# Kernel tuning notes

Measured on AMD Instinct MI355X. Metric: run time of the kernel, lower is better.

Reference implementation:

```python
import jax, jax.numpy as jnp
import numpy as np

EMBED_DIM = 1024
NUM_HEADS = 16
HEAD_DIM = EMBED_DIM // NUM_HEADS
BATCH = 2
SEQ = 2048


def setup_inputs() -> dict:
    key = jax.random.key(0)
    k_x, k_wi, k_bi, k_wo, k_bo = jax.random.split(key, 5)
    scale_in = 1.0 / np.sqrt(EMBED_DIM)
    x = jax.random.normal(k_x, (BATCH, SEQ, EMBED_DIM), dtype=jnp.float32)
    # nn.Linear stores weight [out, in]; we keep [in, out] for x @ W.
    w_in = jax.random.uniform(k_wi, (EMBED_DIM, 3 * EMBED_DIM), jnp.float32, -scale_in, scale_in)
    b_in = jax.random.uniform(k_bi, (3 * EMBED_DIM,), jnp.float32, -scale_in, scale_in)
    w_out = jax.random.uniform(k_wo, (EMBED_DIM, EMBED_DIM), jnp.float32, -scale_in, scale_in)
    b_out = jax.random.uniform(k_bo, (EMBED_DIM,), jnp.float32, -scale_in, scale_in)
    return {"x": x, "w_in": w_in, "b_in": b_in, "w_out": w_out, "b_out": b_out}


def reference(x, w_in, b_in, w_out, b_out):
    B, S, E = x.shape
    H, D = NUM_HEADS, HEAD_DIM
    inp = x @ w_in + b_in                       # [B,S,3E]
    que, key, val = jnp.split(inp, 3, axis=-1)  # each [B,S,E]
    que = que.reshape(B, S, H, D)
    key = key.reshape(B, S, H, D)
    val = val.reshape(B, S, H, D)
    scores = jnp.einsum('bshd,brhd->bhsr', que, key) * (1.0 / np.sqrt(D))
    weights = jax.nn.softmax(scores, axis=-1)   # [B,H,S,S]
    attn = jnp.einsum('bhsr,brhd->bshd', weights, val).reshape(B, S, E)
    return attn @ w_out + b_out
```

## Files before the change

### kernel.cpp

```cpp
#include <hip/hip_runtime.h>


typedef __bf16 bf16x8 __attribute__((ext_vector_type(8)));
typedef float  f32x4  __attribute__((ext_vector_type(4)));
typedef short  s16x4  __attribute__((ext_vector_type(4)));
typedef short  s16x8  __attribute__((ext_vector_type(8)));

__device__ __forceinline__ unsigned short f2b(float f) {
  unsigned u = __float_as_uint(f);
  unsigned r = u + 0x7fffu + ((u >> 16) & 1u);
  return (unsigned short)(r >> 16);
}

__device__ __forceinline__ void gl_lds16(const void* g, void* l) {
  __builtin_amdgcn_global_load_lds(
      (__attribute__((address_space(1))) void*)g,
      (__attribute__((address_space(3))) void*)l, 16, 0, 0);
}

__device__ __forceinline__ f32x4 mfma16x16x16(s16x4 a, s16x4 b, f32x4 c) {
#if defined(__HIP_DEVICE_COMPILE__)
#if __has_builtin(__builtin_amdgcn_mfma_f32_16x16x16bf16_1k)
  return __builtin_amdgcn_mfma_f32_16x16x16bf16_1k(a, b, c, 0, 0, 0);
#else
  s16x8 a8 = {a[0], a[1], a[2], a[3], 0, 0, 0, 0};
  s16x8 b8 = {b[0], b[1], b[2], b[3], 0, 0, 0, 0};
  union U { s16x8 s; bf16x8 v; };
  U ua, ub; ua.s = a8; ub.s = b8;
  return __builtin_amdgcn_mfma_f32_16x16x32_bf16(ua.v, ub.v, c, 0, 0, 0);
#endif
#else
  (void)a; (void)b;
  return c;
#endif
}

__global__ __launch_bounds__(256) void cast_kernel(
    const float* __restrict__ in, unsigned short* __restrict__ out, int n4) {
  int i = blockIdx.x * 256 + threadIdx.x;
  if (i < n4) {
    float4 v = ((const float4*)in)[i];
    ushort4 o;
    o.x = f2b(v.x); o.y = f2b(v.y); o.z = f2b(v.z); o.w = f2b(v.w);
    ((ushort4*)out)[i] = o;
  }
}

__global__ __launch_bounds__(256) void transpose_cast_kernel(
    const float* __restrict__ in, unsigned short* __restrict__ out, int R, int C) {
  __shared__ float tile[64][65];
  int r0 = blockIdx.y * 64, c0 = blockIdx.x * 64;
  int tid = threadIdx.x;
#pragma unroll
  for (int p = 0; p < 16; p++) {
    int i = tid + p * 256;
    int ri = i >> 6, ci = i & 63;
    tile[ri][ci] = in[(size_t)(r0 + ri) * C + c0 + ci];
  }
  __syncthreads();
#pragma unroll
  for (int p = 0; p < 16; p++) {
    int i = tid + p * 256;
    int ci = i >> 6, ri = i & 63;
    out[(size_t)(c0 + ci) * R + r0 + ri] = f2b(tile[ri][ci]);
  }
}

__global__ __launch_bounds__(256) void vt_transpose_kernel(
    const unsigned short* __restrict__ qkv, unsigned short* __restrict__ vt) {
  __shared__ unsigned short tile[64][65];
  int bid = blockIdx.x;
  int st = bid & 31, h = (bid >> 5) & 15, b = bid >> 9;
  int s0 = st * 64;
  int tid = threadIdx.x;
  const unsigned short* src = qkv + (size_t)(b * 2048 + s0) * 3072 + 2048 + h * 64;
#pragma unroll
  for (int p = 0; p < 16; p++) {
    int i = tid + p * 256;
    int sr = i >> 6, d = i & 63;
    tile[sr][d] = src[(size_t)sr * 3072 + d];
  }
  __syncthreads();
  unsigned short* dst = vt + (size_t)(b * 16 + h) * 64 * 2048 + s0;
#pragma unroll
  for (int p = 0; p < 16; p++) {
    int i = tid + p * 256;
    int dr = i >> 6, sc = i & 63;
    dst[(size_t)dr * 2048 + sc] = tile[sc][dr];
  }
}

template <int OUT_BF16>
__global__ __launch_bounds__(256) void gemm_bt(
    const unsigned short* __restrict__ A, const unsigned short* __restrict__ Bt,
    const float* __restrict__ bias, void* __restrict__ Cp, int M, int N, int K,
    int qcols, float qscale) {
  __shared__ __align__(16) unsigned short As[128 * 32];
  __shared__ __align__(16) unsigned short Bs[128 * 32];
  int tid = threadIdx.x;
  int wave = tid >> 6, lane = tid & 63;
  int m_l = lane & 15, quad = lane >> 4;
  int wm = (wave >> 1) * 64, wn = (wave & 1) * 64;
  int row = tid >> 2, kp = (tid & 3) << 3;
  const unsigned short* ag = A + (size_t)(blockIdx.y * 128 + row) * K + kp;
  const unsigned short* bg = Bt + (size_t)(blockIdx.x * 128 + row) * K + kp;
  unsigned short* asw = As + wave * 512;
  unsigned short* bsw = Bs + wave * 512;
  f32x4 acc[4][4] = {};
  for (int k0 = 0; k0 < K; k0 += 32) {
    __syncthreads();
    gl_lds16(ag + k0, asw);
    gl_lds16(ag + (size_t)64 * K + k0, asw + 2048);
    gl_lds16(bg + k0, bsw);
    gl_lds16(bg + (size_t)64 * K + k0, bsw + 2048);
    __syncthreads();
    bf16x8 af[4], bf[4];
#pragma unroll
    for (int i = 0; i < 4; i++)
      af[i] = *(const bf16x8*)&As[(wm + i * 16 + m_l) * 32 + quad * 8];
#pragma unroll
    for (int j = 0; j < 4; j++)
      bf[j] = *(const bf16x8*)&Bs[(wn + j * 16 + m_l) * 32 + quad * 8];
#pragma unroll
    for (int i = 0; i < 4; i++)
#pragma unroll
      for (int j = 0; j < 4; j++)
        acc[i][j] = __builtin_amdgcn_mfma_f32_16x16x32_bf16(af[i], bf[j], acc[i][j], 0, 0, 0);
  }
  float bv[4];
#pragma unroll
  for (int j = 0; j < 4; j++) bv[j] = bias[blockIdx.x * 128 + wn + j * 16 + m_l];
#pragma unroll
  for (int i = 0; i < 4; i++) {
    int m = blockIdx.y * 128 + wm + i * 16 + quad * 4;
#pragma unroll
    for (int j = 0; j < 4; j++) {
      int n = blockIdx.x * 128 + wn + j * 16 + m_l;
      float sc = (OUT_BF16 && n < qcols) ? qscale : 1.0f;
#pragma unroll
      for (int r = 0; r < 4; r++) {
        float v = (acc[i][j][r] + bv[j]) * sc;
        if (OUT_BF16)
          ((unsigned short*)Cp)[(size_t)(m + r) * N + n] = f2b(v);
        else
          ((float*)Cp)[(size_t)(m + r) * N + n] = v;
      }
    }
  }
}

__global__ __launch_bounds__(256) void attn_kernel(
    const unsigned short* __restrict__ qkv, const unsigned short* __restrict__ vt,
    unsigned short* __restrict__ aout) {
  __shared__ __align__(16) unsigned short Qs[128 * 64];
  __shared__ __align__(16) unsigned short Ks[64 * 64];
  __shared__ __align__(16) unsigned short Vts[64 * 64];
  int bid = blockIdx.x;
  int qt = bid & 15, h = (bid >> 4) & 15, b = bid >> 8;
  int tid = threadIdx.x, wave = tid >> 6;
  int lane = tid & 63;
  int m_l = lane & 15, quad = lane >> 4;
  int q0 = qt * 128;
  const unsigned short* qb = qkv + (size_t)b * 2048 * 3072 + h * 64;
  const unsigned short* kb = qb + 1024;
  const unsigned short* vtb = vt + (size_t)(b * 16 + h) * 64 * 2048;

  int srow = tid >> 3;
  int sd0 = ((tid & 7) ^ (srow & 7)) * 8;

#pragma unroll
  for (int i = 0; i < 4; i++)
    gl_lds16(qb + (size_t)(q0 + i * 32 + srow) * 3072 + sd0,
             Qs + wave * 512 + i * 2048);
  __syncthreads();

  int sw0 = ((quad ^ (m_l & 7)) * 8);
  int sw1 = (((quad + 4) ^ (m_l & 7)) * 8);

  bf16x8 qf[2][2];
#pragma unroll
  for (int qi = 0; qi < 2; qi++) {
    int r = (wave * 32 + qi * 16 + m_l) * 64;
    qf[qi][0] = *(const bf16x8*)&Qs[r + sw0];
    qf[qi][1] = *(const bf16x8*)&Qs[r + sw1];
  }

  f32x4 o[2][4] = {};
  float lp[2] = {0.f, 0.f};

  for (int kt = 0; kt < 2048; kt += 64) {
    __syncthreads();
    gl_lds16(kb + (size_t)(kt + srow) * 3072 + sd0, Ks + wave * 512);
    gl_lds16(kb + (size_t)(kt + 32 + srow) * 3072 + sd0, Ks + 2048 + wave * 512);
    gl_lds16(vtb + (size_t)srow * 2048 + kt + sd0, Vts + wave * 512);
    gl_lds16(vtb + (size_t)(32 + srow) * 2048 + kt + sd0, Vts + 2048 + wave * 512);
    __syncthreads();

#pragma unroll
    for (int t = 0; t < 4; t++) {
      int kr = (t * 16 + m_l) * 64;
      bf16x8 kf0 = *(const bf16x8*)&Ks[kr + sw0];
      bf16x8 kf1 = *(const bf16x8*)&Ks[kr + sw1];
      s16x4 pfrag[2];
#pragma unroll
      for (int qi = 0; qi < 2; qi++) {
        f32x4 z = {};
        f32x4 s = __builtin_amdgcn_mfma_f32_16x16x32_bf16(kf0, qf[qi][0], z, 0, 0, 0);
        s = __builtin_amdgcn_mfma_f32_16x16x32_bf16(kf1, qf[qi][1], s, 0, 0, 0);
        float p0 = __builtin_exp2f(s[0]);
        float p1 = __builtin_exp2f(s[1]);
        float p2 = __builtin_exp2f(s[2]);
        float p3 = __builtin_exp2f(s[3]);
        lp[qi] += (p0 + p1) + (p2 + p3);
        s16x4 pk;
        pk[0] = (short)f2b(p0); pk[1] = (short)f2b(p1);
        pk[2] = (short)f2b(p2); pk[3] = (short)f2b(p3);
        pfrag[qi] = pk;
      }
#pragma unroll
      for (int dt = 0; dt < 4; dt++) {
        int drow = dt * 16 + m_l;
        int kchunk = (t * 2 + (quad >> 1)) ^ (m_l & 7);
        s16x4 vf = *(const s16x4*)&Vts[drow * 64 + kchunk * 8 + (quad & 1) * 4];
        o[0][dt] = mfma16x16x16(vf, pfrag[0], o[0][dt]);
        o[1][dt] = mfma16x16x16(vf, pfrag[1], o[1][dt]);
      }
    }
  }

#pragma unroll
  for (int qi = 0; qi < 2; qi++) {
    lp[qi] += __shfl_xor(lp[qi], 16, 64);
    lp[qi] += __shfl_xor(lp[qi], 32, 64);
  }

  unsigned short* ob = aout + (size_t)(b * 2048 + q0 + wave * 32 + m_l) * 1024 +
                       h * 64 + quad * 4;
#pragma unroll
  for (int qi = 0; qi < 2; qi++) {
    float rl = 1.0f / lp[qi];
#pragma unroll
    for (int dt = 0; dt < 4; dt++) {
      ushort4 w;
      w.x = f2b(o[qi][dt][0] * rl);
      w.y = f2b(o[qi][dt][1] * rl);
      w.z = f2b(o[qi][dt][2] * rl);
      w.w = f2b(o[qi][dt][3] * rl);
      *(ushort4*)&ob[(size_t)qi * 16 * 1024 + dt * 16] = w;
    }
  }
}

extern "C" void kernel_launch(void* const* d_in, const int* in_sizes, int n_in,
                              void* d_out, int out_size, void* d_ws, size_t ws_size,
                              hipStream_t stream) {
  (void)in_sizes; (void)n_in; (void)out_size; (void)ws_size;
  const float* x     = (const float*)d_in[0];
  const float* w_in  = (const float*)d_in[1];
  const float* b_in  = (const float*)d_in[2];
  const float* w_out = (const float*)d_in[3];
  const float* b_out = (const float*)d_in[4];
  char* ws = (char*)d_ws;
  unsigned short* xb    = (unsigned short*)(ws + 0);
  unsigned short* wint  = (unsigned short*)(ws + 8388608);
  unsigned short* woutt = (unsigned short*)(ws + 14680064);
  unsigned short* qkv   = (unsigned short*)(ws + 16777216);
  unsigned short* vt    = (unsigned short*)(ws + 41943040);
  unsigned short* attn  = (unsigned short*)(ws + 50331648);
  float* out = (float*)d_out;

  const float QSCALE = 0.125f * 1.44269504088896f;

  cast_kernel<<<4096, 256, 0, stream>>>(x, xb, 1048576);
  transpose_cast_kernel<<<dim3(48, 16), 256, 0, stream>>>(w_in, wint, 1024, 3072);
  transpose_cast_kernel<<<dim3(16, 16), 256, 0, stream>>>(w_out, woutt, 1024, 1024);
  gemm_bt<1><<<dim3(24, 32), 256, 0, stream>>>(xb, wint, b_in, qkv, 4096, 3072, 1024,
                                               1024, QSCALE);
  vt_transpose_kernel<<<1024, 256, 0, stream>>>(qkv, vt);
  attn_kernel<<<512, 256, 0, stream>>>(qkv, vt, attn);
  gemm_bt<0><<<dim3(8, 32), 256, 0, stream>>>(attn, woutt, b_out, out, 4096, 1024, 1024,
                                              0, 1.0f);
}
```

Baseline: 231.7 us.

## Split attention work across 8 waves and use packed bf16 conversion

The attention kernel now launches 512 threads per block, so each of the 8 waves handles 16 query rows instead of 32. K/V tile loads are spread across more threads, which halves the loads issued per thread. The software bf16 rounding is replaced with the hardware v_cvt_pk_bf16_f32 instruction for the probability fragments and the output. This should raise occupancy and latency hiding, but K fragment LDS reads are now amortised over fewer MFMAs per wave, and block-wide barriers cover twice as many waves.

```diff
diff --git a/kernel.cpp b/kernel.cpp
--- a/kernel.cpp
+++ b/kernel.cpp
@@ -10,6 +10,16 @@
   unsigned u = __float_as_uint(f);
   unsigned r = u + 0x7fffu + ((u >> 16) & 1u);
   return (unsigned short)(r >> 16);
+}
+
+__device__ __forceinline__ unsigned cvt_pk_bf16(float a, float b) {
+#if defined(__HIP_DEVICE_COMPILE__)
+  unsigned r;
+  asm("v_cvt_pk_bf16_f32 %0, %1, %2" : "=v"(r) : "v"(a), "v"(b));
+  return r;
+#else
+  return (unsigned)f2b(a) | ((unsigned)f2b(b) << 16);
+#endif
 }
 
 __device__ __forceinline__ void gl_lds16(const void* g, void* l) {
@@ -149,7 +159,7 @@
   }
 }
 
-__global__ __launch_bounds__(256) void attn_kernel(
+__global__ __launch_bounds__(512) void attn_kernel(
     const unsigned short* __restrict__ qkv, const unsigned short* __restrict__ vt,
     unsigned short* __restrict__ aout) {
   __shared__ __align__(16) unsigned short Qs[128 * 64];
@@ -168,32 +178,24 @@
   int srow = tid >> 3;
   int sd0 = ((tid & 7) ^ (srow & 7)) * 8;
 
-#pragma unroll
-  for (int i = 0; i < 4; i++)
-    gl_lds16(qb + (size_t)(q0 + i * 32 + srow) * 3072 + sd0,
-             Qs + wave * 512 + i * 2048);
+  gl_lds16(qb + (size_t)(q0 + srow) * 3072 + sd0, Qs + wave * 512);
+  gl_lds16(qb + (size_t)(q0 + 64 + srow) * 3072 + sd0, Qs + 4096 + wave * 512);
   __syncthreads();
 
   int sw0 = ((quad ^ (m_l & 7)) * 8);
   int sw1 = (((quad + 4) ^ (m_l & 7)) * 8);
 
-  bf16x8 qf[2][2];
-#pragma unroll
-  for (int qi = 0; qi < 2; qi++) {
-    int r = (wave * 32 + qi * 16 + m_l) * 64;
-    qf[qi][0] = *(const bf16x8*)&Qs[r + sw0];
-    qf[qi][1] = *(const bf16x8*)&Qs[r + sw1];
-  }
-
-  f32x4 o[2][4] = {};
-  float lp[2] = {0.f, 0.f};
+  int qrow = (wave * 16 + m_l) * 64;
+  bf16x8 qf0 = *(const bf16x8*)&Qs[qrow + sw0];
+  bf16x8 qf1 = *(const bf16x8*)&Qs[qrow + sw1];
+
+  f32x4 o[4] = {};
+  float lp = 0.f;
 
   for (int kt = 0; kt < 2048; kt += 64) {
     __syncthreads();
     gl_lds16(kb + (size_t)(kt + srow) * 3072 + sd0, Ks + wave * 512);
-    gl_lds16(kb + (size_t)(kt + 32 + srow) * 3072 + sd0, Ks + 2048 + wave * 512);
     gl_lds16(vtb + (size_t)srow * 2048 + kt + sd0, Vts + wave * 512);
-    gl_lds16(vtb + (size_t)(32 + srow) * 2048 + kt + sd0, Vts + 2048 + wave * 512);
     __syncthreads();
 
 #pragma unroll
@@ -201,53 +203,39 @@
       int kr = (t * 16 + m_l) * 64;
       bf16x8 kf0 = *(const bf16x8*)&Ks[kr + sw0];
       bf16x8 kf1 = *(const bf16x8*)&Ks[kr + sw1];
-      s16x4 pfrag[2];
-#pragma unroll
-      for (int qi = 0; qi < 2; qi++) {
-        f32x4 z = {};
-        f32x4 s = __builtin_amdgcn_mfma_f32_16x16x32_bf16(kf0, qf[qi][0], z, 0, 0, 0);
-        s = __builtin_amdgcn_mfma_f32_16x16x32_bf16(kf1, qf[qi][1], s, 0, 0, 0);
-        float p0 = __builtin_exp2f(s[0]);
-        float p1 = __builtin_exp2f(s[1]);
-        float p2 = __builtin_exp2f(s[2]);
-        float p3 = __builtin_exp2f(s[3]);
-        lp[qi] += (p0 + p1) + (p2 + p3);
-        s16x4 pk;
-        pk[0] = (short)f2b(p0); pk[1] = (short)f2b(p1);
-        pk[2] = (short)f2b(p2); pk[3] = (short)f2b(p3);
-        pfrag[qi] = pk;
-      }
+      f32x4 z = {};
+      f32x4 s = __builtin_amdgcn_mfma_f32_16x16x32_bf16(kf0, qf0, z, 0, 0, 0);
+      s = __builtin_amdgcn_mfma_f32_16x16x32_bf16(kf1, qf1, s, 0, 0, 0);
+      float p0 = __builtin_exp2f(s[0]);
+      float p1 = __builtin_exp2f(s[1]);
+      float p2 = __builtin_exp2f(s[2]);
+      float p3 = __builtin_exp2f(s[3]);
+      lp += (p0 + p1) + (p2 + p3);
+      union { uint2 u; s16x4 s4; } pk;
+      pk.u.x = cvt_pk_bf16(p0, p1);
+      pk.u.y = cvt_pk_bf16(p2, p3);
 #pragma unroll
       for (int dt = 0; dt < 4; dt++) {
         int drow = dt * 16 + m_l;
         int kchunk = (t * 2 + (quad >> 1)) ^ (m_l & 7);
         s16x4 vf = *(const s16x4*)&Vts[drow * 64 + kchunk * 8 + (quad & 1) * 4];
-        o[0][dt] = mfma16x16x16(vf, pfrag[0], o[0][dt]);
-        o[1][dt] = mfma16x16x16(vf, pfrag[1], o[1][dt]);
+        o[dt] = mfma16x16x16(vf, pk.s4, o[dt]);
       }
     }
   }
 
-#pragma unroll
-  for (int qi = 0; qi < 2; qi++) {
-    lp[qi] += __shfl_xor(lp[qi], 16, 64);
-    lp[qi] += __shfl_xor(lp[qi], 32, 64);
-  }
-
-  unsigned short* ob = aout + (size_t)(b * 2048 + q0 + wave * 32 + m_l) * 1024 +
+  lp += __shfl_xor(lp, 16, 64);
+  lp += __shfl_xor(lp, 32, 64);
+  float rl = 1.0f / lp;
+
+  unsigned short* ob = aout + (size_t)(b * 2048 + q0 + wave * 16 + m_l) * 1024 +
                        h * 64 + quad * 4;
 #pragma unroll
-  for (int qi = 0; qi < 2; qi++) {
-    float rl = 1.0f / lp[qi];
-#pragma unroll
-    for (int dt = 0; dt < 4; dt++) {
-      ushort4 w;
-      w.x = f2b(o[qi][dt][0] * rl);
-      w.y = f2b(o[qi][dt][1] * rl);
-      w.z = f2b(o[qi][dt][2] * rl);
-      w.w = f2b(o[qi][dt][3] * rl);
-      *(ushort4*)&ob[(size_t)qi * 16 * 1024 + dt * 16] = w;
-    }
+  for (int dt = 0; dt < 4; dt++) {
+    union { uint2 u; ushort4 w; } pk;
+    pk.u.x = cvt_pk_bf16(o[dt][0] * rl, o[dt][1] * rl);
+    pk.u.y = cvt_pk_bf16(o[dt][2] * rl, o[dt][3] * rl);
+    *(ushort4*)&ob[dt * 16] = pk.w;
   }
 }
 
@@ -277,7 +265,7 @@
   gemm_bt<1><<<dim3(24, 32), 256, 0, stream>>>(xb, wint, b_in, qkv, 4096, 3072, 1024,
                                                1024, QSCALE);
   vt_transpose_kernel<<<1024, 256, 0, stream>>>(qkv, vt);
-  attn_kernel<<<512, 256, 0, stream>>>(qkv, vt, attn);
+  attn_kernel<<<512, 512, 0, stream>>>(qkv, vt, attn);
   gemm_bt<0><<<dim3(8, 32), 256, 0, stream>>>(attn, woutt, b_out, out, 4096, 1024, 1024,
                                               0, 1.0f);
 }
```

Result: faster. 215.0 us (-7.2%).
